# Kernel optimization log

Hardware: AMD Instinct MI355X
Metric: run time of the kernel (lower is better)

## Reference

```python
import jax, jax.numpy as jnp
import numpy as np

H = W = 2048

def _conv(x, w, ph, pw):
    # PyTorch Conv2d == cross-correlation, same as lax conv (no kernel flip)
    return jax.lax.conv_general_dilated(
        x, w, (1, 1), [(ph, ph), (pw, pw)],
        dimension_numbers=('NCHW', 'OIHW', 'NCHW'))

def _dir_filters():
    f = np.zeros((8, 1, 3, 3), np.float32)
    f[:, 0, 1, 1] = 1.0
    offs = [(1, 2), (2, 2), (2, 1), (2, 0), (1, 0), (0, 0), (0, 1), (0, 2)]
    for k, (r, c) in enumerate(offs):
        f[k, 0, r, c] = -1.0
    return f

def setup_inputs() -> dict:
    key = jax.random.key(0)
    img = jax.random.uniform(key, (1, 3, H, W), jnp.float32)
    threshold = jnp.ones((1,), jnp.float32)
    # unnormalized scipy.signal.gaussian(5, std=1.0)
    g = np.exp(-0.5 * ((np.arange(5) - 2.0) ** 2)).astype(np.float32)
    gauss_h = jnp.asarray(g.reshape(1, 1, 1, 5))
    gauss_v = jnp.asarray(g.reshape(1, 1, 5, 1))
    sob = np.array([[1, 0, -1], [2, 0, -2], [1, 0, -1]], np.float32)
    sobel_h = jnp.asarray(sob.reshape(1, 1, 3, 3))
    sobel_v = jnp.asarray(sob.T.reshape(1, 1, 3, 3))
    dir_w = jnp.asarray(_dir_filters())
    return dict(img=img, threshold=threshold, gauss_h=gauss_h, gauss_v=gauss_v,
                sobel_h=sobel_h, sobel_v=sobel_v, dir_w=dir_w)

def reference(img, threshold, gauss_h, gauss_v, sobel_h, sobel_v, dir_w):
    def blur(c):
        return _conv(_conv(c, gauss_h, 0, 2), gauss_v, 2, 0)
    br = blur(img[:, 0:1]); bg = blur(img[:, 1:2]); bb = blur(img[:, 2:3])
    blurred_img = jnp.concatenate([br, bg, bb], axis=1)  # [1,3,H,W]
    gx_r = _conv(br, sobel_h, 1, 1); gy_r = _conv(br, sobel_v, 1, 1)
    gx_g = _conv(bg, sobel_h, 1, 1); gy_g = _conv(bg, sobel_v, 1, 1)
    gx_b = _conv(bb, sobel_h, 1, 1); gy_b = _conv(bb, sobel_v, 1, 1)
    grad_mag = (jnp.sqrt(gx_r**2 + gy_r**2)
                + jnp.sqrt(gx_g**2 + gy_g**2)
                + jnp.sqrt(gx_b**2 + gy_b**2))  # [1,1,H,W]
    orient = jnp.arctan2(gy_r + gy_g + gy_b, gx_r + gx_g + gx_b) * (180.0 / 3.14159)
    orient = jnp.round((orient + 180.0) / 45.0) * 45.0  # multiples of 45 in [0,360]
    all_f = _conv(grad_mag, dir_w, 1, 1)  # [1,8,H,W]
    idx_pos = ((orient / 45.0) % 8).astype(jnp.int32)[0, 0]       # [H,W]
    idx_neg = ((orient / 45.0 + 4.0) % 8).astype(jnp.int32)[0, 0]  # [H,W]
    af = all_f[0]  # [8,H,W]
    pos = jnp.take_along_axis(af, idx_pos[None], axis=0)[0]
    neg = jnp.take_along_axis(af, idx_neg[None], axis=0)[0]
    is_max = (jnp.minimum(pos, neg) > 0.0)[None, None]  # [1,1,H,W]
    thin_edges = jnp.where(is_max, grad_mag, 0.0)
    thresholded = jnp.where(thin_edges < threshold, 0.0, thin_edges)
    early_threshold = jnp.where(grad_mag < threshold, 0.0, grad_mag)
    return (blurred_img, grad_mag, orient, thin_edges, thresholded, early_threshold)
```

## Files before the change

kernel.cpp:

```cpp
#include <hip/hip_runtime.h>

#define HH 2048
#define WW 2048
#define HWN (HH * WW)

#define T1F 0.41421317376f
#define T2F 2.41420676750f
#define EPSC 2.0e-5f

#define DYPACK 425u
#define DXPACK 36890u

__device__ __forceinline__ void emit_pixel(
    int py, int px, float gm, float sxf, float syf, float thrf,
    const float (*gmb)[66],
    float* __restrict__ grad, float* __restrict__ orient,
    float* __restrict__ thin, float* __restrict__ thresh,
    float* __restrict__ early)
{
#pragma clang fp contract(fast)
    const size_t idx = (size_t)(blockIdx.y * 16 + py) * WW + (blockIdx.x * 64 + px);

    const float axv = fabsf(sxf), ayv = fabsf(syf);
    const float d1 = ayv - T1F * axv;
    const float d2 = ayv - T2F * axv;
    const float eps = EPSC * (axv + ayv);
    int m;
    if (fabsf(d1) > eps && fabsf(d2) > eps) {
        const bool nx = (__float_as_uint(sxf) >> 31) != 0u;
        const bool ny = (__float_as_uint(syf) >> 31) != 0u;
        if (d1 < 0.0f)      m = nx ? (ny ? 0 : 8) : 4;
        else if (d2 > 0.0f) m = ny ? 2 : 6;
        else                m = nx ? (ny ? 1 : 7) : (ny ? 3 : 5);
    } else {
        const float o = atan2f(syf, sxf) * (float)(180.0 / 3.14159);
        m = (int)rintf((o + 180.0f) / 45.0f);
    }
    const int k = m & 7;
    const int dy = (int)((DYPACK >> (2 * k)) & 3u) - 1;
    const int dx = (int)((DXPACK >> (2 * k)) & 3u) - 1;

    const int r = py + 1, c = px + 1;
    const float gnk  = gmb[r + dy][c + dx];
    const float gnkn = gmb[r - dy][c - dx];
    const float pos = gm - gnk;
    const float neg = gm - gnkn;
    const float mn = fminf(pos, neg);
    const float del = 4.0e-6f * (4.0f + gm + fmaxf(gnk, gnkn));

    float tv;
    if (mn > del)          tv = gm;
    else if (mn < -del)    tv = 0.0f;
    else if (gm < 14.2f)   tv = gm * 0.5f;
    else                   tv = (mn > 0.0f) ? gm : 0.0f;

    grad[idx]   = gm;
    orient[idx] = 45.0f * (float)m;
    early[idx]  = (gm < thrf) ? 0.0f : gm;
    thin[idx]   = tv;
    thresh[idx] = (tv < thrf) ? 0.0f : tv;
}

__device__ __forceinline__ void publish_and_emit(
    float thrf,
    float* __restrict__ grad, float* __restrict__ orient,
    float* __restrict__ thin, float* __restrict__ thresh,
    float* __restrict__ early,
    float (*gmb)[66],
    const float* gmr, const float* sxr, const float* syr,
    float gmt, float sxt, float syt)
{
    const int tx = threadIdx.x;
    const int ty = threadIdx.y;
    const int tid = ty * 64 + tx;

#pragma unroll
    for (int i = 0; i < 5; ++i) {
        const int r = ty + 4 * i;
        if (r < 18) gmb[r][tx] = gmr[i];
    }
    if (tid < 36) gmb[tid >> 1][64 + (tid & 1)] = gmt;
    __syncthreads();

#pragma unroll
    for (int i = 0; i < 5; ++i) {
        const int r = ty + 4 * i;
        if (r >= 1 && r <= 16 && tx >= 1)
            emit_pixel(r - 1, tx - 1, gmr[i], sxr[i], syr[i], thrf, gmb,
                       grad, orient, thin, thresh, early);
    }
    if (tid >= 2 && tid < 34 && (tid & 1) == 0)
        emit_pixel((tid >> 1) - 1, 63, gmt, sxt, syt, thrf, gmb,
                   grad, orient, thin, thresh, early);
}

__device__ void canny_body_edge(
    const float* __restrict__ img, float thrf,
    const float* __restrict__ gh, const float* __restrict__ gv,
    float* __restrict__ blurred,
    float* __restrict__ grad, float* __restrict__ orient,
    float* __restrict__ thin, float* __restrict__ thresh,
    float* __restrict__ early,
    float* bufA, float* bufB, float (*gmb)[66])
{
#pragma clang fp contract(off)
    const int tx = threadIdx.x;
    const int ty = threadIdx.y;
    const int tid = ty * 64 + tx;
    const int x0 = blockIdx.x * 64;
    const int y0 = blockIdx.y * 16;

    float (*raw)[72] = reinterpret_cast<float (*)[72]>(bufA);
    float (*bb)[68]  = reinterpret_cast<float (*)[68]>(bufA);
    float (*hb)[68]  = reinterpret_cast<float (*)[68]>(bufB);

    const float g0 = gh[0], g1 = gh[1], g2 = gh[2], g3 = gh[3], g4 = gh[4];
    const float v0 = gv[0], v1 = gv[1], v2 = gv[2], v3 = gv[3], v4 = gv[4];

    float gmr[5] = {0.f, 0.f, 0.f, 0.f, 0.f};
    float sxr[5] = {0.f, 0.f, 0.f, 0.f, 0.f};
    float syr[5] = {0.f, 0.f, 0.f, 0.f, 0.f};
    float gmt = 0.f, sxt = 0.f, syt = 0.f;

    for (int ch = 0; ch < 3; ++ch) {
        const float* __restrict__ src = img + (size_t)ch * HWN;

        for (int rr = ty; rr < 24; rr += 4) {
            const int gy = y0 - 4 + rr;
            for (int cc = tx; cc < 72; cc += 64) {
                const int gx = x0 - 4 + cc;
                float v = 0.0f;
                if (gy >= 0 && gy < HH && gx >= 0 && gx < WW)
                    v = src[(size_t)gy * WW + gx];
                raw[rr][cc] = v;
            }
        }
        __syncthreads();

        for (int rr = ty; rr < 24; rr += 4) {
            float acc = g0 * raw[rr][tx + 0];
            acc = acc + g1 * raw[rr][tx + 1];
            acc = acc + g2 * raw[rr][tx + 2];
            acc = acc + g3 * raw[rr][tx + 3];
            acc = acc + g4 * raw[rr][tx + 4];
            hb[rr][tx] = acc;
        }
        if (tid < 96) {
            const int rr = tid >> 2, c = 64 + (tid & 3);
            float acc = g0 * raw[rr][c + 0];
            acc = acc + g1 * raw[rr][c + 1];
            acc = acc + g2 * raw[rr][c + 2];
            acc = acc + g3 * raw[rr][c + 3];
            acc = acc + g4 * raw[rr][c + 4];
            hb[rr][c] = acc;
        }
        __syncthreads();

        for (int r = ty; r < 20; r += 4) {
            const int gy = y0 - 2 + r;
            for (int c = tx; c < 68; c += 64) {
                const int gx = x0 - 2 + c;
                float v = 0.0f;
                if (gy >= 0 && gy < HH && gx >= 0 && gx < WW) {
                    float acc = v0 * hb[r + 0][c];
                    acc = acc + v1 * hb[r + 1][c];
                    acc = acc + v2 * hb[r + 2][c];
                    acc = acc + v3 * hb[r + 3][c];
                    acc = acc + v4 * hb[r + 4][c];
                    v = acc;
                }
                bb[r][c] = v;
            }
        }
        __syncthreads();

        {
            float* __restrict__ dst = blurred + (size_t)ch * HWN;
            for (int j = 0; j < 4; ++j) {
                const int rr = ty + 4 * j;
                dst[(size_t)(y0 + rr) * WW + (x0 + tx)] = bb[rr + 2][tx + 2];
            }
        }

#pragma unroll
        for (int i = 0; i < 5; ++i) {
            const int r = ty + 4 * i;
            if (r < 18) {
                const int gy = y0 - 1 + r, gx = x0 - 1 + tx;
                if (gy >= 0 && gy < HH && gx >= 0 && gx < WW) {
                    const float a00 = bb[r][tx],     a01 = bb[r][tx + 1],     a02 = bb[r][tx + 2];
                    const float a10 = bb[r + 1][tx],                          a12 = bb[r + 1][tx + 2];
                    const float a20 = bb[r + 2][tx], a21 = bb[r + 2][tx + 1], a22 = bb[r + 2][tx + 2];
                    const float gxs = (a00 - a02) + 2.0f * (a10 - a12) + (a20 - a22);
                    const float gys = (a00 - a20) + 2.0f * (a01 - a21) + (a02 - a22);
                    gmr[i] = gmr[i] + sqrtf(gxs * gxs + gys * gys);
                    sxr[i] = sxr[i] + gxs;
                    syr[i] = syr[i] + gys;
                }
            }
        }
        if (tid < 36) {
            const int r = tid >> 1, c = 64 + (tid & 1);
            const int gy = y0 - 1 + r, gx = x0 - 1 + c;
            if (gy >= 0 && gy < HH && gx >= 0 && gx < WW) {
                const float a00 = bb[r][c],     a01 = bb[r][c + 1],     a02 = bb[r][c + 2];
                const float a10 = bb[r + 1][c],                         a12 = bb[r + 1][c + 2];
                const float a20 = bb[r + 2][c], a21 = bb[r + 2][c + 1], a22 = bb[r + 2][c + 2];
                const float gxs = (a00 - a02) + 2.0f * (a10 - a12) + (a20 - a22);
                const float gys = (a00 - a20) + 2.0f * (a01 - a21) + (a02 - a22);
                gmt = gmt + sqrtf(gxs * gxs + gys * gys);
                sxt = sxt + gxs;
                syt = syt + gys;
            }
        }
        __syncthreads();
    }

    publish_and_emit(thrf, grad, orient, thin, thresh, early, gmb,
                     gmr, sxr, syr, gmt, sxt, syt);
}

__device__ void canny_body_int(
    const float* __restrict__ img, float thrf,
    const float* __restrict__ gh, const float* __restrict__ gv,
    float* __restrict__ blurred,
    float* __restrict__ grad, float* __restrict__ orient,
    float* __restrict__ thin, float* __restrict__ thresh,
    float* __restrict__ early,
    float* bufA, float* bufB, float (*gmb)[66])
{
#pragma clang fp contract(fast)
    const int tx = threadIdx.x;
    const int ty = threadIdx.y;
    const int tid = ty * 64 + tx;
    const int x0 = blockIdx.x * 64;
    const int y0 = blockIdx.y * 16;

    const float (*raw)[72] = reinterpret_cast<const float (*)[72]>(bufA);
    float (*bb)[68] = reinterpret_cast<float (*)[68]>(bufB);

    const float g0 = gh[0], g1 = gh[1], g2 = gh[2], g3 = gh[3], g4 = gh[4];
    const float v0 = gv[0], v1 = gv[1], v2 = gv[2], v3 = gv[3], v4 = gv[4];

    float gmr[5] = {0.f, 0.f, 0.f, 0.f, 0.f};
    float sxr[5] = {0.f, 0.f, 0.f, 0.f, 0.f};
    float syr[5] = {0.f, 0.f, 0.f, 0.f, 0.f};
    float gmt = 0.f, sxt = 0.f, syt = 0.f;

    const int r0 = tid / 18, c0 = tid - r0 * 18;
    const int t1 = tid + 256;
    const int r1 = t1 / 18, c1 = t1 - r1 * 18;
    const bool has2 = (t1 < 432);
    const size_t tileoff = (size_t)(y0 - 4) * WW + (x0 - 4);

    {
        const float* srow = img + tileoff;
        __builtin_amdgcn_global_load_lds(
            (const __attribute__((address_space(1))) void*)(srow + (size_t)r0 * WW + c0 * 4),
            (__attribute__((address_space(3))) void*)(bufA + tid * 4), 16, 0, 0);
        if (has2)
            __builtin_amdgcn_global_load_lds(
                (const __attribute__((address_space(1))) void*)(srow + (size_t)r1 * WW + c1 * 4),
                (__attribute__((address_space(3))) void*)(bufA + t1 * 4), 16, 0, 0);
    }
    __syncthreads();

    for (int ch = 0; ch < 3; ++ch) {
        {
            const int rbase = 5 * ty;
            float h[9];
#pragma unroll
            for (int kk = 0; kk < 9; ++kk) {
                const float* rp = &raw[rbase + kk][tx];
                h[kk] = g0 * rp[0] + g1 * rp[1] + g2 * rp[2] + g3 * rp[3] + g4 * rp[4];
            }
#pragma unroll
            for (int kk = 0; kk < 5; ++kk)
                bb[rbase + kk][tx] = v0 * h[kk] + v1 * h[kk + 1] + v2 * h[kk + 2]
                                   + v3 * h[kk + 3] + v4 * h[kk + 4];
        }
        if (tid < 16) {
            const int c  = 64 + (tid & 3);
            const int rb = 5 * (tid >> 2);
            float h[9];
#pragma unroll
            for (int kk = 0; kk < 9; ++kk) {
                const float* rp = &raw[rb + kk][c];
                h[kk] = g0 * rp[0] + g1 * rp[1] + g2 * rp[2] + g3 * rp[3] + g4 * rp[4];
            }
#pragma unroll
            for (int kk = 0; kk < 5; ++kk)
                bb[rb + kk][c] = v0 * h[kk] + v1 * h[kk + 1] + v2 * h[kk + 2]
                              + v3 * h[kk + 3] + v4 * h[kk + 4];
        }
        __syncthreads();

        if (ch < 2) {
            const float* srow = img + (size_t)(ch + 1) * HWN + tileoff;
            __builtin_amdgcn_global_load_lds(
                (const __attribute__((address_space(1))) void*)(srow + (size_t)r0 * WW + c0 * 4),
                (__attribute__((address_space(3))) void*)(bufA + tid * 4), 16, 0, 0);
            if (has2)
                __builtin_amdgcn_global_load_lds(
                    (const __attribute__((address_space(1))) void*)(srow + (size_t)r1 * WW + c1 * 4),
                    (__attribute__((address_space(3))) void*)(bufA + t1 * 4), 16, 0, 0);
        }

        {
            float* __restrict__ dst = blurred + (size_t)ch * HWN;
#pragma unroll
            for (int j = 0; j < 4; ++j) {
                const int rr = ty + 4 * j;
                dst[(size_t)(y0 + rr) * WW + (x0 + tx)] = bb[rr + 2][tx + 2];
            }
        }

#pragma unroll
        for (int i = 0; i < 5; ++i) {
            const int r = ty + 4 * i;
            if (r < 18) {
                const float a00 = bb[r][tx],     a01 = bb[r][tx + 1],     a02 = bb[r][tx + 2];
                const float a10 = bb[r + 1][tx],                          a12 = bb[r + 1][tx + 2];
                const float a20 = bb[r + 2][tx], a21 = bb[r + 2][tx + 1], a22 = bb[r + 2][tx + 2];
                const float gxs = (a00 - a02) + 2.0f * (a10 - a12) + (a20 - a22);
                const float gys = (a00 - a20) + 2.0f * (a01 - a21) + (a02 - a22);
                gmr[i] += sqrtf(gxs * gxs + gys * gys);
                sxr[i] += gxs;
                syr[i] += gys;
            }
        }
        if (tid < 36) {
            const int r = tid >> 1, c = 64 + (tid & 1);
            const float a00 = bb[r][c],     a01 = bb[r][c + 1],     a02 = bb[r][c + 2];
            const float a10 = bb[r + 1][c],                         a12 = bb[r + 1][c + 2];
            const float a20 = bb[r + 2][c], a21 = bb[r + 2][c + 1], a22 = bb[r + 2][c + 2];
            const float gxs = (a00 - a02) + 2.0f * (a10 - a12) + (a20 - a22);
            const float gys = (a00 - a20) + 2.0f * (a01 - a21) + (a02 - a22);
            gmt += sqrtf(gxs * gxs + gys * gys);
            sxt += gxs;
            syt += gys;
        }

        if (ch < 2) __syncthreads();
    }

    publish_and_emit(thrf, grad, orient, thin, thresh, early, gmb,
                     gmr, sxr, syr, gmt, sxt, syt);
}

__global__ __launch_bounds__(256) void canny_fused(
    const float* __restrict__ img,
    const float* __restrict__ thrp,
    const float* __restrict__ gh,
    const float* __restrict__ gv,
    float* __restrict__ blurred,
    float* __restrict__ grad,
    float* __restrict__ orient,
    float* __restrict__ thin,
    float* __restrict__ thresh,
    float* __restrict__ early)
{
    __shared__ float bufA[24 * 72];
    __shared__ float bufB[24 * 68];
    __shared__ float gmb[18][66];

    const float thrf = thrp[0];
    const bool edge = (blockIdx.x == 0) | (blockIdx.x == gridDim.x - 1) |
                      (blockIdx.y == 0) | (blockIdx.y == gridDim.y - 1);
    if (edge)
        canny_body_edge(img, thrf, gh, gv, blurred, grad, orient, thin,
                        thresh, early, bufA, bufB, gmb);
    else
        canny_body_int(img, thrf, gh, gv, blurred, grad, orient, thin,
                       thresh, early, bufA, bufB, gmb);
}

extern "C" void kernel_launch(void* const* d_in, const int* in_sizes, int n_in,
                              void* d_out, int out_size, void* d_ws, size_t ws_size,
                              hipStream_t stream)
{
    const float* img = (const float*)d_in[0];
    const float* thr = (const float*)d_in[1];
    const float* gh  = (const float*)d_in[2];
    const float* gv  = (const float*)d_in[3];

    float* out     = (float*)d_out;
    float* blurred = out;
    float* grad    = out + (size_t)3 * HWN;
    float* orient  = out + (size_t)4 * HWN;
    float* thin    = out + (size_t)5 * HWN;
    float* thresh  = out + (size_t)6 * HWN;
    float* early   = out + (size_t)7 * HWN;

    dim3 blk(64, 4, 1);
    dim3 grd(WW / 64, HH / 16, 1);
    canny_fused<<<grd, blk, 0, stream>>>(img, thr, gh, gv,
                                         blurred, grad, orient, thin, thresh, early);
}
```

Baseline: 234.0 us.

## Give each wavefront private LDS slabs to remove block barriers in interior tiles

In interior tiles, each of the four wavefronts now loads its own overlapping row slab of raw input into a private LDS region. It runs the separable blur and Sobel on that slab, so the per-channel __syncthreads and the block-wide global_load_lds prefetch are dropped. The halo column gradients are recomputed redundantly per lane instead of by a separate thread subset, leaving one barrier before the NMS emit. This trades extra redundant halo loads and compute, plus plain per-lane global loads instead of async LDS loads, for fewer barriers and more independence between waves; launch bounds also request 8 blocks per CU.

```diff
diff --git a/kernel.cpp b/kernel.cpp
--- a/kernel.cpp
+++ b/kernel.cpp
@@ -61,7 +61,7 @@
     thresh[idx] = (tv < thrf) ? 0.0f : tv;
 }
 
-__device__ __forceinline__ void publish_and_emit(
+__device__ __forceinline__ void publish_and_emit_edge(
     float thrf,
     float* __restrict__ grad, float* __restrict__ orient,
     float* __restrict__ thin, float* __restrict__ thresh,
@@ -216,8 +216,8 @@
         __syncthreads();
     }
 
-    publish_and_emit(thrf, grad, orient, thin, thresh, early, gmb,
-                     gmr, sxr, syr, gmt, sxt, syt);
+    publish_and_emit_edge(thrf, grad, orient, thin, thresh, early, gmb,
+                          gmr, sxr, syr, gmt, sxt, syt);
 }
 
 __device__ void canny_body_int(
@@ -227,17 +227,23 @@
     float* __restrict__ grad, float* __restrict__ orient,
     float* __restrict__ thin, float* __restrict__ thresh,
     float* __restrict__ early,
-    float* bufA, float* bufB, float (*gmb)[66])
+    float* pool, float (*gmb)[66])
 {
 #pragma clang fp contract(fast)
     const int tx = threadIdx.x;
     const int ty = threadIdx.y;
-    const int tid = ty * 64 + tx;
     const int x0 = blockIdx.x * 64;
     const int y0 = blockIdx.y * 16;
 
-    const float (*raw)[72] = reinterpret_cast<const float (*)[72]>(bufA);
-    float (*bb)[68] = reinterpret_cast<float (*)[68]>(bufB);
+    const int gr0  = (ty < 2) ? 5 * ty : 10 + 4 * (ty - 2);
+    const int ngr  = (ty < 2) ? 5 : 4;
+    const int nbb  = ngr + 2;
+    const int nraw = ngr + 6;
+    const int bl0  = (ty == 0) ? 0 : (ty == 1) ? 4 : (ty == 2) ? 9 : 13;
+    const int nbl  = (ty == 0) ? 4 : (ty == 1) ? 5 : (ty == 2) ? 4 : 3;
+
+    float* rawp = pool + ty * 792;
+    float* bbp  = pool + 3168 + ty * 476;
 
     const float g0 = gh[0], g1 = gh[1], g2 = gh[2], g3 = gh[3], g4 = gh[4];
     const float v0 = gv[0], v1 = gv[1], v2 = gv[2], v3 = gv[3], v4 = gv[4];
@@ -245,110 +251,108 @@
     float gmr[5] = {0.f, 0.f, 0.f, 0.f, 0.f};
     float sxr[5] = {0.f, 0.f, 0.f, 0.f, 0.f};
     float syr[5] = {0.f, 0.f, 0.f, 0.f, 0.f};
-    float gmt = 0.f, sxt = 0.f, syt = 0.f;
-
-    const int r0 = tid / 18, c0 = tid - r0 * 18;
-    const int t1 = tid + 256;
-    const int r1 = t1 / 18, c1 = t1 - r1 * 18;
-    const bool has2 = (t1 < 432);
-    const size_t tileoff = (size_t)(y0 - 4) * WW + (x0 - 4);
-
-    {
-        const float* srow = img + tileoff;
-        __builtin_amdgcn_global_load_lds(
-            (const __attribute__((address_space(1))) void*)(srow + (size_t)r0 * WW + c0 * 4),
-            (__attribute__((address_space(3))) void*)(bufA + tid * 4), 16, 0, 0);
-        if (has2)
-            __builtin_amdgcn_global_load_lds(
-                (const __attribute__((address_space(1))) void*)(srow + (size_t)r1 * WW + c1 * 4),
-                (__attribute__((address_space(3))) void*)(bufA + t1 * 4), 16, 0, 0);
-    }
-    __syncthreads();
+    float gm2[5] = {0.f, 0.f, 0.f, 0.f, 0.f};
 
     for (int ch = 0; ch < 3; ++ch) {
+        const float* __restrict__ src =
+            img + (size_t)ch * HWN + (size_t)(y0 - 4 + gr0) * WW + (x0 - 4);
+
+        for (int r = 0; r < nraw; ++r) {
+            const float* s = src + (size_t)r * WW;
+            rawp[r * 72 + tx] = s[tx];
+            if (tx < 8) rawp[r * 72 + 64 + tx] = s[64 + tx];
+        }
+
         {
-            const int rbase = 5 * ty;
-            float h[9];
-#pragma unroll
-            for (int kk = 0; kk < 9; ++kk) {
-                const float* rp = &raw[rbase + kk][tx];
-                h[kk] = g0 * rp[0] + g1 * rp[1] + g2 * rp[2] + g3 * rp[3] + g4 * rp[4];
-            }
-#pragma unroll
-            for (int kk = 0; kk < 5; ++kk)
-                bb[rbase + kk][tx] = v0 * h[kk] + v1 * h[kk + 1] + v2 * h[kk + 2]
-                                   + v3 * h[kk + 3] + v4 * h[kk + 4];
-        }
-        if (tid < 16) {
-            const int c  = 64 + (tid & 3);
-            const int rb = 5 * (tid >> 2);
-            float h[9];
-#pragma unroll
-            for (int kk = 0; kk < 9; ++kk) {
-                const float* rp = &raw[rb + kk][c];
-                h[kk] = g0 * rp[0] + g1 * rp[1] + g2 * rp[2] + g3 * rp[3] + g4 * rp[4];
-            }
-#pragma unroll
-            for (int kk = 0; kk < 5; ++kk)
-                bb[rb + kk][c] = v0 * h[kk] + v1 * h[kk + 1] + v2 * h[kk + 2]
-                              + v3 * h[kk + 3] + v4 * h[kk + 4];
-        }
-        __syncthreads();
-
-        if (ch < 2) {
-            const float* srow = img + (size_t)(ch + 1) * HWN + tileoff;
-            __builtin_amdgcn_global_load_lds(
-                (const __attribute__((address_space(1))) void*)(srow + (size_t)r0 * WW + c0 * 4),
-                (__attribute__((address_space(3))) void*)(bufA + tid * 4), 16, 0, 0);
-            if (has2)
-                __builtin_amdgcn_global_load_lds(
-                    (const __attribute__((address_space(1))) void*)(srow + (size_t)r1 * WW + c1 * 4),
-                    (__attribute__((address_space(3))) void*)(bufA + t1 * 4), 16, 0, 0);
+            float a0, a1, a2, a3, a4, b0, b1, b2, b3, b4;
+#define HEVAL(hr, HA, HB) do {                                              \
+            const float* rp = &rawp[(hr) * 72 + tx];                        \
+            const float r0_ = rp[0], r1_ = rp[1], r2_ = rp[2], r3_ = rp[3]; \
+            const float r4_ = rp[4], r5_ = rp[5], r6_ = rp[6], r7_ = rp[7]; \
+            const float r8_ = rp[8];                                        \
+            HA = g0 * r0_ + g1 * r1_ + g2 * r2_ + g3 * r3_ + g4 * r4_;      \
+            HB = g0 * r4_ + g1 * r5_ + g2 * r6_ + g3 * r7_ + g4 * r8_;      \
+        } while (0)
+            HEVAL(0, a0, b0); HEVAL(1, a1, b1);
+            HEVAL(2, a2, b2); HEVAL(3, a3, b3);
+#define VSTEP(i) do { if ((i) < nbb) {                                      \
+            HEVAL((i) + 4, a4, b4);                                         \
+            bbp[(i) * 68 + tx] = v0 * a0 + v1 * a1 + v2 * a2                \
+                               + v3 * a3 + v4 * a4;                         \
+            if (tx >= 60)                                                   \
+                bbp[(i) * 68 + tx + 4] = v0 * b0 + v1 * b1 + v2 * b2        \
+                                       + v3 * b3 + v4 * b4;                 \
+            a0 = a1; a1 = a2; a2 = a3; a3 = a4;                             \
+            b0 = b1; b1 = b2; b2 = b3; b3 = b4; } } while (0)
+            VSTEP(0); VSTEP(1); VSTEP(2); VSTEP(3); VSTEP(4); VSTEP(5);
+            { if (6 < nbb) {
+                float a4b, b4b;
+                HEVAL(10, a4b, b4b);
+                bbp[6 * 68 + tx] = v0 * a0 + v1 * a1 + v2 * a2 + v3 * a3 + v4 * a4b;
+                if (tx >= 60)
+                    bbp[6 * 68 + tx + 4] = v0 * b0 + v1 * b1 + v2 * b2 + v3 * b3 + v4 * b4b;
+            } }
+#undef VSTEP
+#undef HEVAL
         }
 
         {
             float* __restrict__ dst = blurred + (size_t)ch * HWN;
-#pragma unroll
-            for (int j = 0; j < 4; ++j) {
-                const int rr = ty + 4 * j;
-                dst[(size_t)(y0 + rr) * WW + (x0 + tx)] = bb[rr + 2][tx + 2];
+            for (int j = 0; j < nbl; ++j) {
+                const int pr = bl0 + j;
+                dst[(size_t)(y0 + pr) * WW + (x0 + tx)] =
+                    bbp[(pr + 2 - gr0) * 68 + tx + 2];
             }
         }
 
 #pragma unroll
         for (int i = 0; i < 5; ++i) {
-            const int r = ty + 4 * i;
-            if (r < 18) {
-                const float a00 = bb[r][tx],     a01 = bb[r][tx + 1],     a02 = bb[r][tx + 2];
-                const float a10 = bb[r + 1][tx],                          a12 = bb[r + 1][tx + 2];
-                const float a20 = bb[r + 2][tx], a21 = bb[r + 2][tx + 1], a22 = bb[r + 2][tx + 2];
-                const float gxs = (a00 - a02) + 2.0f * (a10 - a12) + (a20 - a22);
-                const float gys = (a00 - a20) + 2.0f * (a01 - a21) + (a02 - a22);
+            if (i < ngr) {
+                const float* p0 = &bbp[(i    ) * 68 + tx];
+                const float* p1 = &bbp[(i + 1) * 68 + tx];
+                const float* p2 = &bbp[(i + 2) * 68 + tx];
+                const float w00 = p0[0], w01 = p0[1], w02 = p0[2], w03 = p0[3], w04 = p0[4];
+                const float w10 = p1[0], w11 = p1[1],              w13 = p1[3], w14 = p1[4];
+                const float w20 = p2[0], w21 = p2[1], w22 = p2[2], w23 = p2[3], w24 = p2[4];
+                const float w12 = p1[2];
+                const float gxs = (w01 - w03) + 2.0f * (w11 - w13) + (w21 - w23);
+                const float gys = (w01 - w21) + 2.0f * (w02 - w22) + (w03 - w23);
                 gmr[i] += sqrtf(gxs * gxs + gys * gys);
                 sxr[i] += gxs;
                 syr[i] += gys;
-            }
-        }
-        if (tid < 36) {
-            const int r = tid >> 1, c = 64 + (tid & 1);
-            const float a00 = bb[r][c],     a01 = bb[r][c + 1],     a02 = bb[r][c + 2];
-            const float a10 = bb[r + 1][c],                         a12 = bb[r + 1][c + 2];
-            const float a20 = bb[r + 2][c], a21 = bb[r + 2][c + 1], a22 = bb[r + 2][c + 2];
-            const float gxs = (a00 - a02) + 2.0f * (a10 - a12) + (a20 - a22);
-            const float gys = (a00 - a20) + 2.0f * (a01 - a21) + (a02 - a22);
-            gmt += sqrtf(gxs * gxs + gys * gys);
-            sxt += gxs;
-            syt += gys;
-        }
-
-        if (ch < 2) __syncthreads();
-    }
-
-    publish_and_emit(thrf, grad, orient, thin, thresh, early, gmb,
-                     gmr, sxr, syr, gmt, sxt, syt);
-}
-
-__global__ __launch_bounds__(256) void canny_fused(
+                const bool z = (tx == 0);
+                const float d00 = z ? w00 : w02, d01 = z ? w01 : w03, d02 = z ? w02 : w04;
+                const float d10 = z ? w10 : w12,                      d12 = z ? w12 : w14;
+                const float d20 = z ? w20 : w22, d21 = z ? w21 : w23, d22 = z ? w22 : w24;
+                const float dgx = (d00 - d02) + 2.0f * (d10 - d12) + (d20 - d22);
+                const float dgy = (d00 - d20) + 2.0f * (d01 - d21) + (d02 - d22);
+                gm2[i] += sqrtf(dgx * dgx + dgy * dgy);
+            }
+        }
+    }
+
+#pragma unroll
+    for (int i = 0; i < 5; ++i) {
+        if (i < ngr) {
+            gmb[gr0 + i][tx + 1] = gmr[i];
+            if (tx == 0)  gmb[gr0 + i][0]  = gm2[i];
+            if (tx == 63) gmb[gr0 + i][65] = gm2[i];
+        }
+    }
+    __syncthreads();
+
+#pragma unroll
+    for (int i = 0; i < 5; ++i) {
+        if (i < ngr) {
+            const int g = gr0 + i;
+            if (g >= 1 && g <= 16)
+                emit_pixel(g - 1, tx, gmr[i], sxr[i], syr[i], thrf, gmb,
+                           grad, orient, thin, thresh, early);
+        }
+    }
+}
+
+__global__ __launch_bounds__(256, 8) void canny_fused(
     const float* __restrict__ img,
     const float* __restrict__ thrp,
     const float* __restrict__ gh,
@@ -360,8 +364,7 @@
     float* __restrict__ thresh,
     float* __restrict__ early)
 {
-    __shared__ float bufA[24 * 72];
-    __shared__ float bufB[24 * 68];
+    __shared__ float pool[5072];
     __shared__ float gmb[18][66];
 
     const float thrf = thrp[0];
@@ -369,10 +372,10 @@
                       (blockIdx.y == 0) | (blockIdx.y == gridDim.y - 1);
     if (edge)
         canny_body_edge(img, thrf, gh, gv, blurred, grad, orient, thin,
-                        thresh, early, bufA, bufB, gmb);
+                        thresh, early, pool, pool + 1728, gmb);
     else
         canny_body_int(img, thrf, gh, gv, blurred, grad, orient, thin,
-                       thresh, early, bufA, bufB, gmb);
+                       thresh, early, pool, gmb);
 }
 
 extern "C" void kernel_launch(void* const* d_in, const int* in_sizes, int n_in,
```

Result: slower. 298.0 us (+27.4%).
